# Kernel optimization log

Measured on AMD Instinct MI355X. Metric: run time of the kernel, lower is better.

Reference implementation:

```python
import jax, jax.numpy as jnp
import numpy as np

N_NODES = 50000
N_EDGES = 800000
N_GRAPHS = 256
IN_CH = 128
HID = 256
FFN = 256
OUT = 1


def xavier(key, shape):
    fan_in, fan_out = shape[0], shape[1]
    a = jnp.sqrt(6.0 / (fan_in + fan_out))
    return jax.random.uniform(key, shape, jnp.float32, -a, a)


def setup_inputs() -> dict:
    key = jax.random.key(0)
    ks = jax.random.split(key, 12)
    x = jax.random.normal(ks[0], (N_NODES, IN_CH), jnp.float32)
    edge_index = jax.random.randint(ks[1], (2, N_EDGES), 0, N_NODES, jnp.int32)
    batch = jnp.sort(jax.random.randint(ks[2], (N_NODES,), 0, N_GRAPHS, jnp.int32))
    return {
        "x": x,
        "edge_index": edge_index,
        "batch": batch,
        # GCNConv layers (glorot weight, zero bias as in PyG reset_parameters)
        "W1": xavier(ks[3], (IN_CH, HID)), "b1": jnp.zeros((HID,), jnp.float32),
        "W2": xavier(ks[4], (HID, HID)),   "b2": jnp.zeros((HID,), jnp.float32),
        "W3": xavier(ks[5], (HID, HID)),   "b3": jnp.zeros((HID,), jnp.float32),
        # FFN: Linear(HID, FFN) then final Linear(FFN, OUT)
        "Wf": xavier(ks[6], (HID, FFN)),   "bf": jnp.zeros((FFN,), jnp.float32),
        "Wo": xavier(ks[7], (FFN, OUT)),   "bo": jnp.zeros((OUT,), jnp.float32),
    }


def _gcn_norm(edge_index, n_nodes):
    # add self-loops, compute symmetric normalization D^-1/2 (A+I) D^-1/2
    loops = jnp.arange(n_nodes, dtype=edge_index.dtype)
    row = jnp.concatenate([edge_index[0], loops])
    col = jnp.concatenate([edge_index[1], loops])
    deg = jax.ops.segment_sum(jnp.ones_like(col, jnp.float32), col, num_segments=n_nodes)
    dis = jnp.where(deg > 0, jax.lax.rsqrt(jnp.maximum(deg, 1.0)), 0.0)
    norm = dis[row] * dis[col]  # [E+N]
    return row, col, norm


def _gcn_conv(x, W, b, row, col, norm, n_nodes):
    xw = x @ W                                   # [N, H]
    msg = xw[row] * norm[:, None]                # gather + scale  [E+N, H]
    out = jax.ops.segment_sum(msg, col, num_segments=n_nodes)
    return out + b


def reference(x, edge_index, batch, W1, b1, W2, b2, W3, b3, Wf, bf, Wo, bo):
    row, col, norm = _gcn_norm(edge_index, N_NODES)
    h = jax.nn.relu(_gcn_conv(x, W1, b1, row, col, norm, N_NODES))
    h = jax.nn.relu(_gcn_conv(h, W2, b2, row, col, norm, N_NODES))
    h = jax.nn.relu(_gcn_conv(h, W3, b3, row, col, norm, N_NODES))
    # global mean pool over graphs
    counts = jax.ops.segment_sum(jnp.ones((N_NODES,), jnp.float32), batch, num_segments=N_GRAPHS)
    pooled = jax.ops.segment_sum(h, batch, num_segments=N_GRAPHS) / jnp.maximum(counts, 1.0)[:, None]
    # FFN (dropout is identity in eval mode): Linear -> ReLU -> final Linear
    g = jax.nn.relu(pooled @ Wf + bf)
    out = g @ Wo + bo
    return out
```

## Files before the change

kernel.cpp:

```cpp
#include <hip/hip_runtime.h>
#include <hip/hip_bf16.h>
#include <hip/hip_fp16.h>


#define THREADS 256

typedef _Float16 f16x8 __attribute__((ext_vector_type(8)));
typedef float    f32x4 __attribute__((ext_vector_type(4)));
typedef unsigned short u16x8 __attribute__((ext_vector_type(8)));


__global__ void degree_goff_kernel(const int* __restrict__ col, int* __restrict__ deg, int E,
                                   const int* __restrict__ batch, int* __restrict__ goff,
                                   int N, int G) {
    int i = blockIdx.x * THREADS + threadIdx.x;
    if (i < E) atomicAdd(&deg[col[i]], 1);
    if (i < N) {
        int b1 = batch[i];
        int b0 = (i == 0) ? -1 : batch[i - 1];
        for (int g = b0 + 1; g <= b1; ++g) goff[g] = i;
        if (i == N - 1) {
            for (int g = b1 + 1; g <= G; ++g) goff[g] = N;
        }
    }
}

__global__ __launch_bounds__(256) void scanA_kernel(
    const int* __restrict__ in, int* __restrict__ out, int* __restrict__ bsum,
    float* __restrict__ dis, int n) {
    __shared__ int wsum[4];
    int i0 = blockIdx.x * 1024 + threadIdx.x * 4;
    int lane = threadIdx.x & 63, wid = threadIdx.x >> 6;
    int v0 = 0, v1 = 0, v2 = 0, v3 = 0;
    if (i0 + 3 < n) {
        int4 v = *(const int4*)&in[i0];
        v0 = v.x; v1 = v.y; v2 = v.z; v3 = v.w;
    } else {
        if (i0 + 0 < n) v0 = in[i0 + 0];
        if (i0 + 1 < n) v1 = in[i0 + 1];
        if (i0 + 2 < n) v2 = in[i0 + 2];
        if (i0 + 3 < n) v3 = in[i0 + 3];
    }
    if (i0 + 0 < n) dis[i0 + 0] = rsqrtf((float)(v0 + 1));
    if (i0 + 1 < n) dis[i0 + 1] = rsqrtf((float)(v1 + 1));
    if (i0 + 2 < n) dis[i0 + 2] = rsqrtf((float)(v2 + 1));
    if (i0 + 3 < n) dis[i0 + 3] = rsqrtf((float)(v3 + 1));
    v0 = (v0 + 7) & ~7; v1 = (v1 + 7) & ~7;
    v2 = (v2 + 7) & ~7; v3 = (v3 + 7) & ~7;
    int s = v0 + v1 + v2 + v3;
    int inc = s;
    #pragma unroll
    for (int d = 1; d < 64; d <<= 1) {
        int t = __shfl_up(inc, d);
        if (lane >= d) inc += t;
    }
    if (lane == 63) wsum[wid] = inc;
    __syncthreads();
    int add = 0;
    for (int w = 0; w < wid; ++w) add += wsum[w];
    int ex = add + inc - s;
    if (i0 + 0 < n) out[i0 + 0] = ex;
    if (i0 + 1 < n) out[i0 + 1] = ex + v0;
    if (i0 + 2 < n) out[i0 + 2] = ex + v0 + v1;
    if (i0 + 3 < n) out[i0 + 3] = ex + v0 + v1 + v2;
    if (threadIdx.x == 255) bsum[blockIdx.x] = add + inc;
}

__global__ void scanB_kernel(int* __restrict__ bsum, int* __restrict__ total_slot, int nb) {
    int lane = threadIdx.x;
    int v = (lane < nb) ? bsum[lane] : 0;
    int inc = v;
    #pragma unroll
    for (int d = 1; d < 64; d <<= 1) {
        int t = __shfl_up(inc, d);
        if (lane >= d) inc += t;
    }
    if (lane < nb) bsum[lane] = inc - v;
    if (lane == 63) *total_slot = inc;
}

__global__ __launch_bounds__(256) void slicecnt_kernel(
    const int* __restrict__ deg, int* __restrict__ scnt, int N) {
    __shared__ int wsum[4];
    int s = blockIdx.x;
    int SL = (N + 7) >> 3;
    int lo = s * SL, hi = min(N, lo + SL);
    int acc = 0;
    for (int i = lo + (int)threadIdx.x; i < hi; i += 256) acc += deg[i];
    #pragma unroll
    for (int d = 1; d < 64; d <<= 1) acc += __shfl_xor(acc, d);
    int lane = threadIdx.x & 63, wid = threadIdx.x >> 6;
    if (lane == 0) wsum[wid] = acc;
    __syncthreads();
    if (threadIdx.x == 0) scnt[s] = wsum[0] + wsum[1] + wsum[2] + wsum[3];
}

__global__ void scan8_kernel(const int* __restrict__ scnt, int* __restrict__ binoff,
                             int* __restrict__ bcur) {
    if (threadIdx.x == 0 && blockIdx.x == 0) {
        int cum = 0;
        for (int s = 0; s < 8; ++s) { binoff[s] = cum; bcur[s] = cum; cum += scnt[s]; }
        binoff[8] = cum;
    }
}

__global__ __launch_bounds__(256) void translate_bin_kernel(
    const int* __restrict__ row, const int* __restrict__ col,
    unsigned int* __restrict__ bins, int* __restrict__ bcur, int E, int N) {
    __shared__ unsigned int lent[2048];
    __shared__ int lhist[8], lbase[8], gbase[8], lpos[8];
    int t = threadIdx.x;
    if (t < 8) lhist[t] = 0;
    __syncthreads();
    int SL = (N + 7) >> 3;
    int e0 = blockIdx.x * 2048 + t * 8;
    unsigned int ent[8]; int sl[8];
    int n = E - e0; if (n < 0) n = 0; if (n > 8) n = 8;
    if (n == 8) {
        int4 c0 = *(const int4*)&col[e0];
        int4 c1 = *(const int4*)&col[e0 + 4];
        int4 r0 = *(const int4*)&row[e0];
        int4 r1 = *(const int4*)&row[e0 + 4];
        int cs[8] = {c0.x, c0.y, c0.z, c0.w, c1.x, c1.y, c1.z, c1.w};
        int rs[8] = {r0.x, r0.y, r0.z, r0.w, r1.x, r1.y, r1.z, r1.w};
        #pragma unroll
        for (int j = 0; j < 8; ++j) {
            sl[j] = cs[j] / SL;
            ent[j] = (unsigned int)cs[j] | ((unsigned int)rs[j] << 16);
            atomicAdd(&lhist[sl[j]], 1);
        }
    } else {
        for (int j = 0; j < n; ++j) {
            int c = col[e0 + j], r = row[e0 + j];
            sl[j] = c / SL;
            ent[j] = (unsigned int)c | ((unsigned int)r << 16);
            atomicAdd(&lhist[sl[j]], 1);
        }
    }
    __syncthreads();
    if (t == 0) {
        int cum = 0;
        #pragma unroll
        for (int s = 0; s < 8; ++s) { lbase[s] = cum; cum += lhist[s]; }
    }
    __syncthreads();
    if (t < 8) { gbase[t] = atomicAdd(&bcur[t], lhist[t]); lpos[t] = lbase[t]; }
    __syncthreads();
    for (int j = 0; j < n; ++j) {
        int p = atomicAdd(&lpos[sl[j]], 1);
        lent[p] = ent[j];
    }
    __syncthreads();
    int total = lbase[7] + lhist[7];
    for (int k = t; k < total; k += 256) {
        unsigned int e = lent[k];
        int s = 0;
        #pragma unroll
        for (int b = 1; b < 8; ++b) s = (k >= lbase[b]) ? b : s;
        bins[gbase[s] + (k - lbase[s])] = e;
    }
}

__global__ __launch_bounds__(256) void padfill_x_kernel(
    const int* __restrict__ offs, const int* __restrict__ deg,
    unsigned short* __restrict__ srcs, int N) {
    int slice = blockIdx.x & 7;
    int SL = (N + 7) >> 3;
    int node = slice * SL + (int)(blockIdx.x >> 3) * THREADS + threadIdx.x;
    int nhi = min(N, slice * SL + SL);
    if (node >= nhi) return;
    int s = offs[node] + deg[node], e = offs[node + 1];
    for (int i = s; i < e; ++i) srcs[i] = (unsigned short)N;
}

__global__ __launch_bounds__(256) void csr_fill2_kernel(
    const unsigned int* __restrict__ bins, const int* __restrict__ binoff,
    const int* __restrict__ offs, int* __restrict__ deg,
    unsigned short* __restrict__ srcs, int CPS) {
    int slice = blockIdx.x & 7;
    int chunk = blockIdx.x >> 3;
    int lo = binoff[slice], hi = binoff[slice + 1];
    for (int base = lo + chunk * 2048; base < hi; base += CPS * 2048) {
        int i0 = base + (int)threadIdx.x * 8;
        #pragma unroll
        for (int j = 0; j < 8; ++j) {
            int i = i0 + j;
            if (i < hi) {
                unsigned int e = bins[i];
                int c = (int)(e & 0xffffu);
                int r = (int)(e >> 16);
                int old = atomicSub(&deg[c], 1);
                srcs[offs[c] + old - 1] = (unsigned short)r;
            }
        }
    }
}

__global__ void convert_kernel(
    int* __restrict__ offs, const int* __restrict__ bsum, int Nfix,
    const float* __restrict__ X, const float* __restrict__ dis,
    _Float16* __restrict__ Xs, int total8, int IC,
    const float* __restrict__ W1, _Float16* __restrict__ W1t, int k1,
    const float* __restrict__ W2, _Float16* __restrict__ W2t,
    const float* __restrict__ W3, _Float16* __restrict__ W3t,
    _Float16* __restrict__ Hs) {
    int i = blockIdx.x * THREADS + threadIdx.x;
    if (i < Nfix) {
        offs[i] += bsum[i >> 10];
        return;
    }
    int j = i - Nfix;
    int Ms = Nfix + 1;
    if (j < total8) {
        int idx = j * 8;
        int node = idx / IC;
        int ch0  = idx % IC;
        float d = dis[node];
        float4 a = *(const float4*)&X[idx];
        float4 b = *(const float4*)&X[idx + 4];
        f16x8 o;
        o[0] = (_Float16)(d * a.x); o[1] = (_Float16)(d * a.y);
        o[2] = (_Float16)(d * a.z); o[3] = (_Float16)(d * a.w);
        o[4] = (_Float16)(d * b.x); o[5] = (_Float16)(d * b.y);
        o[6] = (_Float16)(d * b.z); o[7] = (_Float16)(d * b.w);
        int sw = IC >> 3;
        int slice = ch0 / sw, within = ch0 % sw;
        *(f16x8*)&Xs[((size_t)slice * Ms + node) * sw + within] = o;
        return;
    }
    j -= total8;
    int n1 = k1 * 256;
    if (j < n1) {
        int k = j >> 8, n = j & 255;
        W1t[n * k1 + k] = (_Float16)W1[j];
        return;
    }
    j -= n1;
    if (j < 65536) {
        int k = j >> 8, n = j & 255;
        W2t[n * 256 + k] = (_Float16)W2[j];
        return;
    }
    j -= 65536;
    if (j < 65536) {
        int k = j >> 8, n = j & 255;
        W3t[n * 256 + k] = (_Float16)W3[j];
        return;
    }
    j -= 65536;
    {
        int swx = IC >> 3;
        int nx = 8 * swx;
        if (j < nx) {
            int slice = j / swx, wi = j % swx;
            Xs[((size_t)slice * Ms + Nfix) * swx + wi] = (_Float16)0.f;
            return;
        }
        j -= nx;
        if (j < 256) {
            int slice = j >> 5, wi = j & 31;
            Hs[((size_t)slice * Ms + Nfix) * 32 + wi] = (_Float16)0.f;
        }
    }
}


template<int CH>
__global__ __launch_bounds__(256) void aggregate_slice_kernel(
    const _Float16* __restrict__ X, const int* __restrict__ offs,
    const unsigned short* __restrict__ srcs, const float* __restrict__ dis,
    _Float16* __restrict__ A, int N) {
    constexpr int LPN = CH / 64;
    constexpr int NPB = 256 / LPN;
    int bid   = blockIdx.x;
    int slice = bid & 7;
    int tile  = bid >> 3;
    int node  = tile * NPB + threadIdx.x / LPN;
    if (node >= N) return;
    int lane = threadIdx.x % LPN;
    size_t Ms = (size_t)N + 1;
    const f16x8* Xv = (const f16x8*)X + (size_t)slice * Ms * LPN;
    f16x8 self = Xv[(size_t)node * LPN + lane];
    float acc[8], acc2[8];
    #pragma unroll
    for (int j = 0; j < 8; ++j) { acc[j] = (float)self[j]; acc2[j] = 0.f; }
    int s = offs[node], e = offs[node + 1];
    int nit = (e - s) >> 3;
    if (nit > 0) {
        const u16x8* ip = (const u16x8*)&srcs[s];
        u16x8 idx = ip[0];
        for (int it = 0; it < nit; ++it) {
            u16x8 nxt = ip[min(it + 1, nit - 1)];
            f16x8 v0 = Xv[(size_t)idx[0] * LPN + lane];
            f16x8 v1 = Xv[(size_t)idx[1] * LPN + lane];
            f16x8 v2 = Xv[(size_t)idx[2] * LPN + lane];
            f16x8 v3 = Xv[(size_t)idx[3] * LPN + lane];
            f16x8 v4 = Xv[(size_t)idx[4] * LPN + lane];
            f16x8 v5 = Xv[(size_t)idx[5] * LPN + lane];
            f16x8 v6 = Xv[(size_t)idx[6] * LPN + lane];
            f16x8 v7 = Xv[(size_t)idx[7] * LPN + lane];
            #pragma unroll
            for (int j = 0; j < 8; ++j) {
                acc[j]  += ((float)v0[j] + (float)v2[j]) + ((float)v4[j] + (float)v6[j]);
                acc2[j] += ((float)v1[j] + (float)v3[j]) + ((float)v5[j] + (float)v7[j]);
            }
            idx = nxt;
        }
    }
    float dn = dis[node];
    f16x8 o;
    #pragma unroll
    for (int j = 0; j < 8; ++j) o[j] = (_Float16)(dn * (acc[j] + acc2[j]));
    f16x8* Av = (f16x8*)A + (size_t)slice * Ms * LPN;
    __builtin_nontemporal_store(o, &Av[(size_t)node * LPN + lane]);
}


template<int K, int MODE>
__global__ __launch_bounds__(256) void gemm_as_kernel(
    const _Float16* __restrict__ A, const _Float16* __restrict__ Bt,
    const float* __restrict__ bias, const float* __restrict__ dscale,
    _Float16* __restrict__ H, float* __restrict__ pooled,
    const int* __restrict__ batch, int M, int Ms) {
    constexpr int LSA = K + 40;
    constexpr int KC = K / 32;
    constexpr int SPR = K / 8;
    constexpr int SPS = K / 64;
    constexpr int SW  = K / 8;
    __shared__ _Float16 As[64 * LSA];
    int tid = threadIdx.x;
    int m0 = blockIdx.x * 64;

    {
        constexpr int RPI = 256 / SPR;
        int r_in = tid % RPI;
        int seg  = tid / RPI;
        int slice = seg / SPS, sub = seg % SPS;
        #pragma unroll
        for (int it = 0; it < 64 / RPI; ++it) {
            int r = it * RPI + r_in;
            int gr = m0 + r;
            uint4 v = make_uint4(0, 0, 0, 0);
            if (gr < M) v = *(const uint4*)&A[((size_t)slice * Ms + gr) * SW + sub * 8];
            *(uint4*)&As[r * LSA + seg * 8] = v;
        }
    }
    __syncthreads();

    int wid = tid >> 6, lane = tid & 63;
    int l16 = lane & 15, quad = lane >> 4;
    int wn = wid * 64;

    f32x4 acc[4][4] = {};
    const _Float16* Bbase = Bt + (size_t)(wn + l16) * K + quad * 8;

    #pragma unroll
    for (int kc = 0; kc < KC; ++kc) {
        f16x8 bh[4];
        #pragma unroll
        for (int ni = 0; ni < 4; ++ni)
            bh[ni] = *(const f16x8*)&Bbase[(size_t)(ni * 16) * K + kc * 32];
        #pragma unroll
        for (int mi = 0; mi < 4; ++mi) {
            f16x8 ah = *(const f16x8*)&As[(mi * 16 + l16) * LSA + kc * 32 + quad * 8];
            #pragma unroll
            for (int ni = 0; ni < 4; ++ni)
                acc[mi][ni] = __builtin_amdgcn_mfma_f32_16x16x32_f16(ah, bh[ni], acc[mi][ni], 0, 0, 0);
        }
    }

    #pragma unroll
    for (int mi = 0; mi < 4; ++mi) {
        int rbase = m0 + mi * 16;
        int g0 = 0, g15 = 0;
        if (MODE == 2) {
            g0  = batch[min(rbase, M - 1)];
            g15 = batch[min(rbase + 15, M - 1)];
        }
        #pragma unroll
        for (int ni = 0; ni < 4; ++ni) {
            int col = wn + ni * 16 + l16;
            float bv = bias[col];
            if (MODE == 1) {
                size_t hbase = (size_t)(col >> 5) * Ms * 32 + (col & 31);
                #pragma unroll
                for (int r = 0; r < 4; ++r) {
                    int grow = rbase + quad * 4 + r;
                    if (grow < M) {
                        float v = fmaxf(acc[mi][ni][r] + bv, 0.f) * dscale[grow];
                        H[hbase + (size_t)grow * 32] = (_Float16)v;
                    }
                }
            } else {
                if (g0 == g15) {
                    float p = 0.f;
                    #pragma unroll
                    for (int r = 0; r < 4; ++r) {
                        int grow = rbase + quad * 4 + r;
                        float v = fmaxf(acc[mi][ni][r] + bv, 0.f);
                        p += (grow < M) ? v : 0.f;
                    }
                    p += __shfl_xor(p, 16);
                    p += __shfl_xor(p, 32);
                    if (quad == 0) atomicAdd(&pooled[g0 * 256 + col], p);
                } else {
                    #pragma unroll
                    for (int r = 0; r < 4; ++r) {
                        int grow = rbase + quad * 4 + r;
                        if (grow < M) {
                            float v = fmaxf(acc[mi][ni][r] + bv, 0.f);
                            atomicAdd(&pooled[batch[grow] * 256 + col], v);
                        }
                    }
                }
            }
        }
    }
}


__global__ __launch_bounds__(256) void ffn_kernel(
    const float* __restrict__ pooled, const int* __restrict__ goff,
    const float* __restrict__ Wf, const float* __restrict__ bf,
    const float* __restrict__ Wo, const float* __restrict__ bo,
    float* __restrict__ out) {
    __shared__ float p[256];
    __shared__ float red[256];
    int g = blockIdx.x, t = threadIdx.x;
    int cnt = goff[g + 1] - goff[g];
    float inv = 1.f / (float)max(cnt, 1);
    p[t] = pooled[g * 256 + t] * inv;
    __syncthreads();
    float s = bf[t];
    #pragma unroll 8
    for (int k = 0; k < 256; ++k) s = fmaf(p[k], Wf[k * 256 + t], s);
    float gv = fmaxf(s, 0.f);
    red[t] = gv * Wo[t];
    __syncthreads();
    for (int o = 128; o > 0; o >>= 1) {
        if (t < o) red[t] += red[t + o];
        __syncthreads();
    }
    if (t == 0) out[g] = red[0] + bo[0];
}


extern "C" void kernel_launch(void* const* d_in, const int* in_sizes, int n_in,
                              void* d_out, int out_size, void* d_ws, size_t ws_size,
                              hipStream_t stream) {
    const float* x   = (const float*)d_in[0];
    const int*   ei  = (const int*)d_in[1];
    const int*   bat = (const int*)d_in[2];
    const float* W1  = (const float*)d_in[3];
    const float* b1  = (const float*)d_in[4];
    const float* W2  = (const float*)d_in[5];
    const float* b2  = (const float*)d_in[6];
    const float* W3  = (const float*)d_in[7];
    const float* b3  = (const float*)d_in[8];
    const float* Wf  = (const float*)d_in[9];
    const float* bf  = (const float*)d_in[10];
    const float* Wo  = (const float*)d_in[11];
    const float* bo  = (const float*)d_in[12];
    float* out = (float*)d_out;

    const int N  = in_sizes[2];
    const int E  = in_sizes[1] / 2;
    const int IC = in_sizes[0] / N;
    const int HID = 256;
    const int G  = out_size;
    const int Ms = N + 1;
    const int* row = ei;
    const int* col = ei + E;

    char* w = (char*)d_ws;
    size_t off = 0;
    auto alloc = [&](size_t bytes) -> void* {
        void* p = w + off;
        off += (bytes + 255) & ~(size_t)255;
        return p;
    };
    int*   deg    = (int*)alloc((size_t)N * 4);
    float* pooled = (float*)alloc((size_t)G * HID * 4);
    float* dis    = (float*)alloc((size_t)N * 4);
    int*   offs   = (int*)alloc((size_t)(N + 1) * 4);
    unsigned short* srcs = (unsigned short*)alloc(((size_t)E + 7 * (size_t)N + 8) * 2);
    unsigned int* bins = (unsigned int*)alloc((size_t)(E + 8) * 4);
    int*   scnt   = (int*)alloc((size_t)8 * 4);
    int*   binoff = (int*)alloc((size_t)9 * 4);
    int*   bcur   = (int*)alloc((size_t)8 * 4);
    int*   goff   = (int*)alloc((size_t)(G + 1) * 4);
    int*   bsum   = (int*)alloc((size_t)64 * 4);
    _Float16* W1t = (_Float16*)alloc((size_t)HID * IC * 2);
    _Float16* W2t = (_Float16*)alloc((size_t)HID * HID * 2);
    _Float16* W3t = (_Float16*)alloc((size_t)HID * HID * 2);
    _Float16* Xs  = (_Float16*)alloc((size_t)Ms * IC * 2);
    _Float16* Ah  = (_Float16*)alloc((size_t)Ms * HID * 2);
    _Float16* Hs  = (_Float16*)alloc((size_t)Ms * HID * 2);
    (void)ws_size; (void)n_in;

    size_t zlen = (((size_t)N * 4 + 255) & ~(size_t)255) + (size_t)G * HID * 4;
    hipMemsetAsync(deg, 0, zlen, stream);

    degree_goff_kernel<<<(E + THREADS - 1) / THREADS, THREADS, 0, stream>>>(
        col, deg, E, bat, goff, N, G);

    int nb = (N + 1023) / 1024;
    scanA_kernel<<<nb, 256, 0, stream>>>(deg, offs, bsum, dis, N);
    scanB_kernel<<<1, 64, 0, stream>>>(bsum, &offs[N], nb);

    slicecnt_kernel<<<8, 256, 0, stream>>>(deg, scnt, N);
    scan8_kernel<<<1, 64, 0, stream>>>(scnt, binoff, bcur);
    translate_bin_kernel<<<(E + 2047) / 2048, 256, 0, stream>>>(
        row, col, bins, bcur, E, N);

    int total8 = N * IC / 8;
    int conv_total = N + total8 + IC * HID + HID * HID + HID * HID + 8 * (IC / 8) + 256;
    convert_kernel<<<(conv_total + THREADS - 1) / THREADS, THREADS, 0, stream>>>(
        offs, bsum, N, x, dis, Xs, total8, IC, W1, W1t, IC, W2, W2t, W3, W3t, Hs);

    int SL = (N + 7) >> 3;
    int pf_tiles = (SL + THREADS - 1) / THREADS;
    padfill_x_kernel<<<pf_tiles * 8, THREADS, 0, stream>>>(offs, deg, srcs, N);
    int CPS = (E + 8 * 2048 - 1) / (8 * 2048);
    csr_fill2_kernel<<<CPS * 8, 256, 0, stream>>>(bins, binoff, offs, deg, srcs, CPS);

    int mtiles = (N + 63) / 64;
    int nt1 = (N + 127) / 128;
    aggregate_slice_kernel<128><<<nt1 * 8, 256, 0, stream>>>(Xs, offs, srcs, dis, Ah, N);
    gemm_as_kernel<128, 1><<<mtiles, 256, 0, stream>>>(Ah, W1t, b1, dis, Hs, nullptr, nullptr, N, Ms);
    int nt2 = (N + 63) / 64;
    aggregate_slice_kernel<256><<<nt2 * 8, 256, 0, stream>>>(Hs, offs, srcs, dis, Ah, N);
    gemm_as_kernel<256, 1><<<mtiles, 256, 0, stream>>>(Ah, W2t, b2, dis, Hs, nullptr, nullptr, N, Ms);
    aggregate_slice_kernel<256><<<nt2 * 8, 256, 0, stream>>>(Hs, offs, srcs, dis, Ah, N);
    gemm_as_kernel<256, 2><<<mtiles, 256, 0, stream>>>(Ah, W3t, b3, nullptr, nullptr, pooled, bat, N, Ms);

    ffn_kernel<<<G, 256, 0, stream>>>(pooled, goff, Wf, bf, Wo, bo, out);
}
```

Measured before the change: 410.7 us.

## Sort nodes into degree buckets to balance per-wave work in aggregation

```diff
diff --git a/kernel.cpp b/kernel.cpp
--- a/kernel.cpp
+++ b/kernel.cpp
@@ -22,6 +22,32 @@
         if (i == N - 1) {
             for (int g = b1 + 1; g <= G; ++g) goff[g] = N;
         }
+    }
+}
+
+__global__ void bucketcnt_kernel(const int* __restrict__ deg, int* __restrict__ bcnt, int N) {
+    int i = blockIdx.x * THREADS + threadIdx.x;
+    if (i < N) atomicAdd(&bcnt[min((deg[i] + 7) >> 3, 63)], 1);
+}
+
+__global__ void bucketscan_kernel(int* __restrict__ b) {
+    int lane = threadIdx.x;
+    int v = b[lane];
+    int inc = v;
+    #pragma unroll
+    for (int d = 1; d < 64; d <<= 1) {
+        int t = __shfl_up(inc, d);
+        if (lane >= d) inc += t;
+    }
+    b[lane] = inc - v;
+}
+
+__global__ void place_kernel(const int* __restrict__ deg, int* __restrict__ bcnt,
+                             int* __restrict__ order, int N) {
+    int i = blockIdx.x * THREADS + threadIdx.x;
+    if (i < N) {
+        int pos = atomicAdd(&bcnt[min((deg[i] + 7) >> 3, 63)], 1);
+        order[pos] = i;
     }
 }
 
@@ -269,14 +295,15 @@
 __global__ __launch_bounds__(256) void aggregate_slice_kernel(
     const _Float16* __restrict__ X, const int* __restrict__ offs,
     const unsigned short* __restrict__ srcs, const float* __restrict__ dis,
-    _Float16* __restrict__ A, int N) {
+    const int* __restrict__ order, _Float16* __restrict__ A, int N) {
     constexpr int LPN = CH / 64;
     constexpr int NPB = 256 / LPN;
     int bid   = blockIdx.x;
     int slice = bid & 7;
     int tile  = bid >> 3;
-    int node  = tile * NPB + threadIdx.x / LPN;
-    if (node >= N) return;
+    int slot  = tile * NPB + threadIdx.x / LPN;
+    if (slot >= N) return;
+    int node = order[slot];
     int lane = threadIdx.x % LPN;
     size_t Ms = (size_t)N + 1;
     const f16x8* Xv = (const f16x8*)X + (size_t)slice * Ms * LPN;
@@ -312,7 +339,7 @@
     #pragma unroll
     for (int j = 0; j < 8; ++j) o[j] = (_Float16)(dn * (acc[j] + acc2[j]));
     f16x8* Av = (f16x8*)A + (size_t)slice * Ms * LPN;
-    __builtin_nontemporal_store(o, &Av[(size_t)node * LPN + lane]);
+    Av[(size_t)node * LPN + lane] = o;
 }
 
 
@@ -481,6 +508,7 @@
     };
     int*   deg    = (int*)alloc((size_t)N * 4);
     float* pooled = (float*)alloc((size_t)G * HID * 4);
+    int*   bcnt   = (int*)alloc((size_t)64 * 4);
     float* dis    = (float*)alloc((size_t)N * 4);
     int*   offs   = (int*)alloc((size_t)(N + 1) * 4);
     unsigned short* srcs = (unsigned short*)alloc(((size_t)E + 7 * (size_t)N + 8) * 2);
@@ -490,6 +518,7 @@
     int*   bcur   = (int*)alloc((size_t)8 * 4);
     int*   goff   = (int*)alloc((size_t)(G + 1) * 4);
     int*   bsum   = (int*)alloc((size_t)64 * 4);
+    int*   order  = (int*)alloc((size_t)N * 4);
     _Float16* W1t = (_Float16*)alloc((size_t)HID * IC * 2);
     _Float16* W2t = (_Float16*)alloc((size_t)HID * HID * 2);
     _Float16* W3t = (_Float16*)alloc((size_t)HID * HID * 2);
@@ -498,11 +527,18 @@
     _Float16* Hs  = (_Float16*)alloc((size_t)Ms * HID * 2);
     (void)ws_size; (void)n_in;
 
-    size_t zlen = (((size_t)N * 4 + 255) & ~(size_t)255) + (size_t)G * HID * 4;
+    size_t zlen = (((size_t)N * 4 + 255) & ~(size_t)255)
+                + (((size_t)G * HID * 4 + 255) & ~(size_t)255)
+                + (size_t)64 * 4;
     hipMemsetAsync(deg, 0, zlen, stream);
 
     degree_goff_kernel<<<(E + THREADS - 1) / THREADS, THREADS, 0, stream>>>(
         col, deg, E, bat, goff, N, G);
+
+    int nblk = (N + THREADS - 1) / THREADS;
+    bucketcnt_kernel<<<nblk, THREADS, 0, stream>>>(deg, bcnt, N);
+    bucketscan_kernel<<<1, 64, 0, stream>>>(bcnt);
+    place_kernel<<<nblk, THREADS, 0, stream>>>(deg, bcnt, order, N);
 
     int nb = (N + 1023) / 1024;
     scanA_kernel<<<nb, 256, 0, stream>>>(deg, offs, bsum, dis, N);
@@ -526,12 +562,12 @@
 
     int mtiles = (N + 63) / 64;
     int nt1 = (N + 127) / 128;
-    aggregate_slice_kernel<128><<<nt1 * 8, 256, 0, stream>>>(Xs, offs, srcs, dis, Ah, N);
+    aggregate_slice_kernel<128><<<nt1 * 8, 256, 0, stream>>>(Xs, offs, srcs, dis, order, Ah, N);
     gemm_as_kernel<128, 1><<<mtiles, 256, 0, stream>>>(Ah, W1t, b1, dis, Hs, nullptr, nullptr, N, Ms);
     int nt2 = (N + 63) / 64;
-    aggregate_slice_kernel<256><<<nt2 * 8, 256, 0, stream>>>(Hs, offs, srcs, dis, Ah, N);
+    aggregate_slice_kernel<256><<<nt2 * 8, 256, 0, stream>>>(Hs, offs, srcs, dis, order, Ah, N);
     gemm_as_kernel<256, 1><<<mtiles, 256, 0, stream>>>(Ah, W2t, b2, dis, Hs, nullptr, nullptr, N, Ms);
-    aggregate_slice_kernel<256><<<nt2 * 8, 256, 0, stream>>>(Hs, offs, srcs, dis, Ah, N);
+    aggregate_slice_kernel<256><<<nt2 * 8, 256, 0, stream>>>(Hs, offs, srcs, dis, order, Ah, N);
     gemm_as_kernel<256, 2><<<mtiles, 256, 0, stream>>>(Ah, W3t, b3, nullptr, nullptr, pooled, bat, N, Ms);
 
     ffn_kernel<<<G, 256, 0, stream>>>(pooled, goff, Wf, bf, Wo, bo, out);
```

Result: slower. 1.188 ms (+189.4%).
